# Optimization experiments

Measured on AMD Instinct MI355X. Metric: run time of the kernel, lower is better.

Reference implementation:

```python
import jax, jax.numpy as jnp
import numpy as np

B, T, HOR, N = 32, 12, 12, 883
D = 10      # embed_dim == time_dim
HID = 64    # rnn_units
OUT = 1     # output_dim
K = 2       # cheb_k: supports [I, A]


def _pdg2(x, e1, e2, E, Wp, bp):
    # x:[B,N,Ci]  e1,e2:[B,N,D]  E:[N,D]  Wp:[D,K,Ci,Co]  bp:[D,Co]
    nv1 = jnp.tanh(E[None] * e1)                      # [B,N,D]
    nv2 = jnp.tanh(E[None] * e2)
    A = jax.nn.softmax(jax.nn.relu(jnp.einsum('bnd,bmd->bnm', nv1, nv2)), axis=-1)
    xg = jnp.stack([x, jnp.einsum('bnm,bmc->bnc', A, x)], axis=2)   # [B,N,K,Ci]
    W = jnp.einsum('bnd,dkio->bnkio', nv1, Wp)        # node/time-adaptive weights
    b = jnp.einsum('bnd,do->bno', nv1, bp)
    return jnp.einsum('bnki,bnkio->bno', xg, W) + b


def _cell(x, h, e1, e2, E, gW, gb, uW, ub):
    xs = jnp.concatenate([x, h], axis=-1)
    zr = jax.nn.sigmoid(_pdg2(xs, e1, e2, E, gW, gb))
    z, r = jnp.split(zr, 2, axis=-1)
    cand = jnp.concatenate([x, z * h], axis=-1)
    hc = jnp.tanh(_pdg2(cand, e1, e2, E, uW, ub))
    return r * h + (1.0 - r) * hc


def setup_inputs() -> dict:
    key = jax.random.key(0)
    ks = jax.random.split(key, 20)
    s = 0.1
    inp = {
        'src_vals': jax.random.normal(ks[0], (B, T, N, 1), jnp.float32),
        'node_emb': s * jax.random.normal(ks[1], (N, D), jnp.float32),
        'tid_emb1': s * jax.random.normal(ks[2], (288, D), jnp.float32),
        'tid_emb2': s * jax.random.normal(ks[3], (288, D), jnp.float32),
        'diw_emb1': s * jax.random.normal(ks[4], (7, D), jnp.float32),
        'diw_emb2': s * jax.random.normal(ks[5], (7, D), jnp.float32),
        'enc_gate_W': s * jax.random.normal(ks[6], (D, K, 1 + HID, 2 * HID), jnp.float32),
        'enc_gate_b': s * jax.random.normal(ks[7], (D, 2 * HID), jnp.float32),
        'enc_upd_W': s * jax.random.normal(ks[8], (D, K, 1 + HID, HID), jnp.float32),
        'enc_upd_b': s * jax.random.normal(ks[9], (D, HID), jnp.float32),
        'dec_gate_W': s * jax.random.normal(ks[10], (D, K, OUT + HID, 2 * HID), jnp.float32),
        'dec_gate_b': s * jax.random.normal(ks[11], (D, 2 * HID), jnp.float32),
        'dec_upd_W': s * jax.random.normal(ks[12], (D, K, OUT + HID, HID), jnp.float32),
        'dec_upd_b': s * jax.random.normal(ks[13], (D, HID), jnp.float32),
        'proj_W': s * jax.random.normal(ks[14], (OUT, HID), jnp.float32),
        'proj_b': jnp.zeros((OUT,), jnp.float32),
        'src_tid': jax.random.randint(ks[15], (B, T, N), 0, 288, jnp.int32),
        'src_diw': jax.random.randint(ks[16], (B, T, N), 0, 7, jnp.int32),
        'tgt_tid': jax.random.randint(ks[17], (B, HOR, N), 0, 288, jnp.int32),
        'tgt_diw': jax.random.randint(ks[18], (B, HOR, N), 0, 7, jnp.int32),
    }
    return inp


def reference(src_vals, node_emb, tid_emb1, tid_emb2, diw_emb1, diw_emb2,
              enc_gate_W, enc_gate_b, enc_upd_W, enc_upd_b,
              dec_gate_W, dec_gate_b, dec_upd_W, dec_upd_b,
              proj_W, proj_b, src_tid, src_diw, tgt_tid, tgt_diw):
    tm = lambda a: jnp.swapaxes(a, 0, 1)   # batch-major -> time-major
    # periodic embeddings (use_week=True -> elementwise product)
    e1_en = tid_emb1[src_tid] * diw_emb1[src_diw]   # [B,T,N,D]
    e2_en = tid_emb2[src_tid] * diw_emb2[src_diw]
    e1_de = tid_emb1[tgt_tid] * diw_emb1[tgt_diw]   # [B,HOR,N,D]
    e2_de = tid_emb2[tgt_tid] * diw_emb2[tgt_diw]

    h0 = jnp.zeros((src_vals.shape[0], node_emb.shape[0], HID), src_vals.dtype)

    def enc_step(h, inp):
        x, e1, e2 = inp
        h = _cell(x, h, e1, e2, node_emb, enc_gate_W, enc_gate_b, enc_upd_W, enc_upd_b)
        return h, None

    h, _ = jax.lax.scan(enc_step, h0, (tm(src_vals), tm(e1_en), tm(e2_en)))

    go0 = jnp.zeros((src_vals.shape[0], node_emb.shape[0], OUT), src_vals.dtype)

    def dec_step(carry, inp):
        h, go = carry
        e1, e2 = inp
        h = _cell(go, h, e1, e2, node_emb, dec_gate_W, dec_gate_b, dec_upd_W, dec_upd_b)
        go = h @ proj_W.T + proj_b
        return (h, go), go

    _, outs = jax.lax.scan(dec_step, (h, go0), (tm(e1_de), tm(e2_de)))
    return jnp.swapaxes(outs, 0, 1)   # [B,HOR,N,OUT]
```

## Files before the change

### kernel.cpp

```cpp
#include <hip/hip_runtime.h>

#define BB 32
#define TSRC 12
#define HORZ 12
#define NN 883
#define DD 10
#define HH 64
#define BN (BB*NN)
#define BNP 28288
#define KF 5
#define NT 14

typedef __attribute__((ext_vector_type(8))) short short8;
typedef __attribute__((ext_vector_type(4))) float f32x4;

static __device__ __forceinline__ float sigmf(float x) { return 1.f/(1.f + __expf(-x)); }
static __device__ __forceinline__ float tanh_fast(float x) {
  float e = __expf(2.f*x);
  return (e - 1.f) / (e + 1.f);
}
static __device__ __forceinline__ unsigned int bf_hi(float f) {
  unsigned int u = __float_as_uint(f);
  return (u + 0x7fffu + ((u >> 16) & 1u)) >> 16;
}
static __device__ __forceinline__ float bf_f(unsigned int h) {
  return __uint_as_float(h << 16);
}
static __device__ __forceinline__ void lds_load16(const void* g, void* l) {
  __builtin_amdgcn_global_load_lds(
      (const __attribute__((address_space(1))) void*)g,
      (__attribute__((address_space(3))) void*)l, 16, 0, 0);
}

static __device__ __forceinline__ void swz_block(int& b, int& rt) {
  int lin = blockIdx.x + blockIdx.y*NT;
  int c = lin & 7, q = lin >> 3;
  b = c + ((q/NT) << 3);
  rt = q - (q/NT)*NT;
}

static __device__ __forceinline__ void xs_store(unsigned short* chunk, int c, int mm2, float v) {
  int p0 = (c*128 + (mm2 ^ ((c & 7) << 4))) >> 1;
  unsigned int hi = bf_hi(v);
  chunk[p0] = (unsigned short)hi;
  chunk[p0 + 4096] = (unsigned short)bf_hi(v - bf_f(hi));
}

__global__ __launch_bounds__(256) void prep_kernel(
    const float* __restrict__ tidE1, const float* __restrict__ tidE2,
    const float* __restrict__ diwE1, const float* __restrict__ diwE2,
    const float* __restrict__ nodeE,
    const int* __restrict__ tididx, const int* __restrict__ diwidx,
    const float* __restrict__ xsrc, int xmode, int t, int tlen,
    float* __restrict__ nv1T, float* __restrict__ nv2T,
    unsigned short* __restrict__ XsH, unsigned short* __restrict__ XsZ)
{
  int i = blockIdx.x*256 + threadIdx.x;
  if (i >= BN) return;
  int b = i / NN, n = i - b*NN;
  int gi = (b*tlen + t)*NN + n;
  int ti = tididx[gi]*DD, di = diwidx[gi]*DD;
  int nE = n*DD;
#pragma unroll
  for (int d = 0; d < DD; ++d) {
    float E = nodeE[nE+d];
    nv1T[d*BNP+i] = tanh_fast(E * (tidE1[ti+d] * diwE1[di+d]));
    nv2T[d*BNP+i] = tanh_fast(E * (tidE2[ti+d] * diwE2[di+d]));
  }
  float xv = (xmode == 0) ? xsrc[gi] : xsrc[i];
  size_t cb = ((size_t)(b*NT + (n >> 6)))*8192;
  int mm = n & 63;
  unsigned int hi = bf_hi(xv);
  unsigned short los = (unsigned short)bf_hi(xv - bf_f(hi));
  XsH[cb + mm] = (unsigned short)hi; XsH[cb + 4096 + mm] = los;
  XsZ[cb + mm] = (unsigned short)hi; XsZ[cb + 4096 + mm] = los;
}

__global__ __launch_bounds__(256) void wsplit_kernel(
    const float* __restrict__ W, const float* __restrict__ bias,
    int NO, unsigned short* __restrict__ Wf)
{
  int i = blockIdx.x*256 + threadIdx.x;
  int total = DD*2*KF*4*NO*8;
  if (i >= total) return;
  int j = i & 7; int r = i >> 3;
  int o = r % NO; r /= NO;
  int quad = r & 3; r >>= 2;
  int kf = r % KF; r /= KF;
  int hl = r & 1; int d = r >> 1;
  int kk = kf*32 + quad*8 + j;
  float v = 0.f;
  if (kk <= 64)       v = W[(size_t)(d*130 + kk)*NO + o];
  else if (kk == 65)  v = bias[d*NO + o];
  else if (kk <= 130) v = W[(size_t)(d*130 + kk - 1)*NO + o];
  unsigned int hi = bf_hi(v);
  Wf[i] = (hl == 0) ? (unsigned short)hi : (unsigned short)bf_hi(v - bf_f(hi));
}


__global__ __launch_bounds__(256,3) void attn_gate(
    const float* __restrict__ nv1T, const float* __restrict__ nv2T,
    const unsigned short* __restrict__ Xs,
    const float* __restrict__ h,
    const unsigned short* __restrict__ Wf,
    float* __restrict__ rbuf,
    unsigned short* __restrict__ XsZ, float* __restrict__ zh63)
{
  __shared__ float nv1s[DD][64];
  __shared__ float linv[64];
  __shared__ alignas(16) unsigned char U[46080];
  unsigned short* XT = (unsigned short*)U;
  unsigned short* PT = (unsigned short*)(U + 16384);
  float* nv2s = (float*)(U + 34816);
  float* xcolb = (float*)(U + 39936);
  int b, rt;
  swz_block(b, rt);
  int r0 = rt*64;
  int tid = threadIdx.x;
  int rg = tid >> 4, cg = tid & 15;
  int base = b*NN;
  int lane = tid & 63, lm = lane & 15, quad = lane >> 4;
  int w = tid >> 6, mp = w >> 1, np = w & 1;
  const unsigned short* XsB = Xs + (size_t)b*NT*8192;

  for (int idx = tid; idx < DD*64; idx += 256) {
    int d = idx >> 6, r = idx & 63;
    nv1s[d][r] = (r0 + r < NN) ? nv1T[d*BNP + base + r0 + r] : 0.f;
  }

  int4 xt[4];
  float nvr[3]; float xcr;
  {
    const int4* s0 = (const int4*)XsB;
#pragma unroll
    for (int i = 0; i < 4; ++i) xt[i] = s0[w*64 + lane + i*256];
#pragma unroll
    for (int i = 0; i < 3; ++i) {
      int idx = tid + i*256; float v = 0.f;
      if (idx < DD*64) { int d = idx>>6, m = idx&63; v = (m < NN) ? nv2T[d*BNP + base + m] : 0.f; }
      nvr[i] = v;
    }
    xcr = (tid < 64 && tid < NN) ? h[(size_t)63*BNP + base + tid] : 0.f;
#pragma unroll
    for (int i = 0; i < 4; ++i)
      *(int4*)((char*)XT + w*1024 + lane*16 + i*4096) = xt[i];
#pragma unroll
    for (int i = 0; i < 3; ++i) {
      int idx = tid + i*256;
      if (idx < DD*64) nv2s[idx] = nvr[i];
    }
    if (tid < 64) xcolb[tid] = xcr;
  }
  __syncthreads();

  f32x4 accv[2][2] = {};
  float acclp[4] = {}, acc5p[4] = {};

  for (int tI = 0; tI < NT; ++tI) {
    int cur = tI & 1, nxt = cur ^ 1;
    int m0 = tI*64, m0n = m0 + 64;
    bool hasn = tI < NT-1;
    if (hasn) {
      const int4* src = (const int4*)(XsB + (size_t)(tI+1)*8192);
#pragma unroll
      for (int i = 0; i < 4; ++i) xt[i] = src[w*64 + lane + i*256];
#pragma unroll
      for (int i = 0; i < 3; ++i) {
        int idx = tid + i*256; float v = 0.f;
        if (idx < DD*64) { int d = idx>>6, m = idx&63; v = (m0n + m < NN) ? nv2T[d*BNP + base + m0n + m] : 0.f; }
        nvr[i] = v;
      }
      xcr = (tid < 64 && m0n + tid < NN) ? h[(size_t)63*BNP + base + m0n + tid] : 0.f;
    }
    float s[4][4] = {};
#pragma unroll
    for (int d = 0; d < DD; ++d) {
      float4 a4 = *(const float4*)&nv1s[d][rg*4];
      float4 c4 = *(const float4*)&nv2s[cur*(DD*64) + d*64 + cg*4];
      const float* ap = (const float*)&a4;
      const float* cp = (const float*)&c4;
#pragma unroll
      for (int j = 0; j < 4; ++j)
#pragma unroll
        for (int jj = 0; jj < 4; ++jj)
          s[j][jj] += ap[j]*cp[jj];
    }
    int mvlim = NN - m0;
    float ev[4][4];
#pragma unroll
    for (int jj = 0; jj < 4; ++jj) {
      int m = cg*4 + jj;
      float xm = xcolb[cur*64 + m];
      bool okm = m < mvlim;
#pragma unroll
      for (int j = 0; j < 4; ++j) {
        float e = okm ? __expf(fmaxf(s[j][jj], 0.f)) : 0.f;
        ev[j][jj] = e;
        acclp[j] += e;
        acc5p[j] = fmaf(e, xm, acc5p[j]);
      }
    }
    {
      unsigned int* P1 = (unsigned int*)PT;
      unsigned int* P2 = (unsigned int*)(PT + 64*72);
#pragma unroll
      for (int j = 0; j < 4; ++j) {
        int r = rg*4 + j;
        unsigned int h0 = bf_hi(ev[j][0]), h1 = bf_hi(ev[j][1]), h2 = bf_hi(ev[j][2]), h3 = bf_hi(ev[j][3]);
        unsigned int l0 = bf_hi(ev[j][0]-bf_f(h0)), l1 = bf_hi(ev[j][1]-bf_f(h1));
        unsigned int l2 = bf_hi(ev[j][2]-bf_f(h2)), l3 = bf_hi(ev[j][3]-bf_f(h3));
        int dw = r*36 + cg*2;
        P1[dw] = h0 | (h1 << 16); P1[dw+1] = h2 | (h3 << 16);
        P2[dw] = l0 | (l1 << 16); P2[dw+1] = l2 | (l3 << 16);
      }
    }
    __syncthreads();
    {
      short8 Aa[2][2], Ab[2][2], Ba[2][2], Bb[2][2];
#pragma unroll
      for (int mt = 0; mt < 2; ++mt) {
        int r = mp*32 + mt*16 + lm;
#pragma unroll
        for (int kf = 0; kf < 2; ++kf) {
          Aa[mt][kf] = *(const short8*)&PT[r*72 + quad*8 + kf*32];
          Ab[mt][kf] = *(const short8*)&PT[64*72 + r*72 + quad*8 + kf*32];
        }
      }
#pragma unroll
      for (int ntl = 0; ntl < 2; ++ntl) {
        int c = np*32 + ntl*16 + lm;
        int swz = (c & 7) << 4;
        int cb0 = c*128 + quad*16;
#pragma unroll
        for (int kf = 0; kf < 2; ++kf) {
          int a = (cb0 + kf*64) ^ swz;
          Ba[ntl][kf] = *(const short8*)((const char*)XT + a);
          Bb[ntl][kf] = *(const short8*)((const char*)XT + a + 8192);
        }
      }
#pragma unroll
      for (int kf = 0; kf < 2; ++kf)
#pragma unroll
        for (int mt = 0; mt < 2; ++mt)
#pragma unroll
          for (int ntl = 0; ntl < 2; ++ntl) {
            accv[mt][ntl] = __builtin_amdgcn_mfma_f32_16x16x32_bf16(Aa[mt][kf], Ba[ntl][kf], accv[mt][ntl], 0,0,0);
            accv[mt][ntl] = __builtin_amdgcn_mfma_f32_16x16x32_bf16(Aa[mt][kf], Bb[ntl][kf], accv[mt][ntl], 0,0,0);
            accv[mt][ntl] = __builtin_amdgcn_mfma_f32_16x16x32_bf16(Ab[mt][kf], Ba[ntl][kf], accv[mt][ntl], 0,0,0);
          }
    }
    if (hasn) {
#pragma unroll
      for (int i = 0; i < 3; ++i) {
        int idx = tid + i*256;
        if (idx < DD*64) nv2s[nxt*(DD*64) + idx] = nvr[i];
      }
      if (tid < 64) xcolb[nxt*64 + tid] = xcr;
    }
    __syncthreads();
    if (hasn) {
#pragma unroll
      for (int i = 0; i < 4; ++i)
        *(int4*)((char*)XT + w*1024 + lane*16 + i*4096) = xt[i];
    }
  }
  int mrow_x = tid >> 2, ksub = tid & 3;
  int gmx = base + r0 + mrow_x;
  const unsigned short* chk_in = Xs + (size_t)(b*NT + rt)*8192;
  int mm2x = mrow_x*2;
  unsigned int pjh[9], pjl[9];
  {
    float r63v = h[(size_t)63*BNP + gmx];
    unsigned int h63 = bf_hi(r63v);
    unsigned int l63 = bf_hi(r63v - bf_f(h63));
#pragma unroll
    for (int i = 0; i < 9; ++i) {
      int kk = ksub*2 + 8*i;
      unsigned int h0 = 0, l0 = 0, h1 = 0, l1 = 0;
      if (kk <= 63) {
        int idx = (kk*128 + (mm2x ^ ((kk & 7) << 4))) >> 1;
        h0 = chk_in[idx]; l0 = chk_in[idx + 4096];
      } else if (kk == 64) { h0 = h63; l0 = l63; }
      int k1 = kk + 1;
      if (kk <= 62) {
        int idx1 = (k1*128 + (mm2x ^ ((k1 & 7) << 4))) >> 1;
        h1 = chk_in[idx1]; l1 = chk_in[idx1 + 4096];
      } else if (k1 == 65) { h1 = 0x3F80u; l1 = 0u; }
      pjh[i] = h0 | (h1 << 16);
      pjl[i] = l0 | (l1 << 16);
    }
  }
#pragma unroll
  for (int off = 1; off <= 8; off <<= 1)
#pragma unroll
    for (int j = 0; j < 4; ++j) {
      acclp[j] += __shfl_xor(acclp[j], off, 64);
      acc5p[j] += __shfl_xor(acc5p[j], off, 64);
    }
  __syncthreads();
  {
    unsigned int* Z = (unsigned int*)(U + 36864);
    for (int idx = tid; idx < 2304; idx += 256) Z[idx] = 0;
  }
  __syncthreads();
  unsigned short* XA = (unsigned short*)U;
  if (cg == 0) {
#pragma unroll
    for (int j = 0; j < 4; ++j) {
      float li = 1.f / acclp[j];
      int r = rg*4 + j;
      linv[r] = li;
      float v = acc5p[j]*li;
      unsigned int hi = bf_hi(v);
      XA[(4*64 + r)*72 + 2] = (unsigned short)hi;
      XA[(4*64 + r)*72 + 32 + 2] = (unsigned short)bf_hi(v - bf_f(hi));
    }
  }
  __syncthreads();
#pragma unroll
  for (int mt = 0; mt < 2; ++mt) {
    int rbase = mp*32 + mt*16 + quad*4;
    float4 lv = *(const float4*)&linv[rbase];
    const float* lvp = (const float*)&lv;
#pragma unroll
    for (int ntl = 0; ntl < 2; ++ntl) {
      int c = np*32 + ntl*16 + lm;
      int kk = 66 + c;
      int kf = kk >> 5, kkl = kk & 31;
#pragma unroll
      for (int r4 = 0; r4 < 4; ++r4) {
        float v = accv[mt][ntl][r4] * lvp[r4];
        unsigned int hi = bf_hi(v);
        int p = (kf*64 + rbase + r4)*72 + kkl;
        XA[p] = (unsigned short)hi;
        XA[p + 32] = (unsigned short)bf_hi(v - bf_f(hi));
      }
    }
  }
  {
    unsigned int* X1 = (unsigned int*)U;
#pragma unroll
    for (int i = 0; i < 9; ++i) {
      int kk = ksub*2 + 8*i;
      if (kk > 64) continue;
      int kf = kk >> 5, kkl = kk & 31;
      int dw = (kf*64 + mrow_x)*36 + (kkl >> 1);
      X1[dw] = pjh[i];
      X1[dw + 16] = pjl[i];
    }
  }
  __syncthreads();
  short8 A1[2][KF], A2[2][KF];
#pragma unroll
  for (int mt = 0; mt < 2; ++mt) {
    int mrow = mp*32 + mt*16 + lm;
#pragma unroll
    for (int kf = 0; kf < KF; ++kf) {
      A1[mt][kf] = *(const short8*)&XA[(kf*64 + mrow)*72 + quad*8];
      A2[mt][kf] = *(const short8*)&XA[(kf*64 + mrow)*72 + 32 + quad*8];
    }
  }
  __syncthreads();
  unsigned char* bufA = U;
  unsigned char* bufB = U + 20480;
  const int colb = np*32 + lm;
#pragma unroll 1
  for (int co = 0; co < 2; ++co) {
    int co0 = co*64;
    {
      const unsigned short* src = Wf + ((size_t)(w*5)*128 + co0)*8 + lane*8;
#pragma unroll
      for (int i = 0; i < 5; ++i)
        lds_load16(src + (size_t)i*128*8, bufA + (w*5+i)*1024);
    }
    f32x4 accO[2][2] = {};
#pragma unroll 1
    for (int d = 0; d < DD; ++d) {
      f32x4 td[2][2] = {};
      __syncthreads();
      {
        const unsigned short* src = Wf + ((size_t)((d*2+1)*20 + w*5)*128 + co0)*8 + lane*8;
#pragma unroll
        for (int i = 0; i < 5; ++i)
          lds_load16(src + (size_t)i*128*8, bufB + (w*5+i)*1024);
      }
#pragma unroll
      for (int kf = 0; kf < KF; ++kf) {
        int cb = ((kf*4 + quad)*64 + colb)*16;
#pragma unroll
        for (int ntl = 0; ntl < 2; ++ntl) {
          short8 Bh = *(const short8*)(bufA + cb + ntl*256);
          td[0][ntl] = __builtin_amdgcn_mfma_f32_16x16x32_bf16(A1[0][kf], Bh, td[0][ntl], 0,0,0);
          td[0][ntl] = __builtin_amdgcn_mfma_f32_16x16x32_bf16(A2[0][kf], Bh, td[0][ntl], 0,0,0);
          td[1][ntl] = __builtin_amdgcn_mfma_f32_16x16x32_bf16(A1[1][kf], Bh, td[1][ntl], 0,0,0);
          td[1][ntl] = __builtin_amdgcn_mfma_f32_16x16x32_bf16(A2[1][kf], Bh, td[1][ntl], 0,0,0);
        }
      }
      __syncthreads();
      if (d < DD-1) {
        const unsigned short* src = Wf + ((size_t)((d+1)*2*20 + w*5)*128 + co0)*8 + lane*8;
#pragma unroll
        for (int i = 0; i < 5; ++i)
          lds_load16(src + (size_t)i*128*8, bufA + (w*5+i)*1024);
      }
#pragma unroll
      for (int kf = 0; kf < KF; ++kf) {
        int cb = ((kf*4 + quad)*64 + colb)*16;
#pragma unroll
        for (int ntl = 0; ntl < 2; ++ntl) {
          short8 Bl = *(const short8*)(bufB + cb + ntl*256);
          td[0][ntl] = __builtin_amdgcn_mfma_f32_16x16x32_bf16(A1[0][kf], Bl, td[0][ntl], 0,0,0);
          td[1][ntl] = __builtin_amdgcn_mfma_f32_16x16x32_bf16(A1[1][kf], Bl, td[1][ntl], 0,0,0);
        }
      }
#pragma unroll
      for (int mt = 0; mt < 2; ++mt) {
        float4 nv4 = *(const float4*)&nv1s[d][mp*32 + mt*16 + quad*4];
        const float* nvp = (const float*)&nv4;
#pragma unroll
        for (int ntl = 0; ntl < 2; ++ntl)
#pragma unroll
          for (int r = 0; r < 4; ++r)
            accO[mt][ntl][r] += nvp[r] * td[mt][ntl][r];
      }
    }
    float* CT = (float*)U;
    __syncthreads();
#pragma unroll
    for (int mt = 0; mt < 2; ++mt)
#pragma unroll
      for (int ntl = 0; ntl < 2; ++ntl)
#pragma unroll
        for (int r = 0; r < 4; ++r)
          CT[(mp*32 + mt*16 + quad*4 + r)*67 + np*32 + ntl*16 + lm] = accO[mt][ntl][r];
    __syncthreads();
    {
      int mm = tid & 63, og = tid >> 6;
      int n = r0 + mm;
      int gm = base + n;
      bool okn = n < NN;
      if (co == 0) {
        unsigned short* chk = XsZ + ((size_t)(b*NT + rt))*8192;
        int mm2 = mm*2;
        for (int j = 0; j < 16; ++j) {
          int o = og*16 + j;
          float z = sigmf(CT[mm*67 + o]);
          float zhv = z * h[(size_t)o*BNP + gm];
          if (okn) {
            if (o < 63) xs_store(chk, o + 1, mm2, zhv);
            else zh63[gm] = zhv;
          }
        }
      } else {
        for (int j = 0; j < 16; ++j) {
          int o = og*16 + j;
          if (okn) rbuf[(size_t)o*BNP + gm] = sigmf(CT[mm*67 + o]);
        }
      }
    }
    __syncthreads();
  }
}

__global__ __launch_bounds__(256,3) void attn_upd(
    const float* __restrict__ nv1T, const float* __restrict__ nv2T,
    const unsigned short* __restrict__ Xs,
    const float* __restrict__ zh63,
    float* __restrict__ hstate,
    const unsigned short* __restrict__ Wf,
    const float* __restrict__ rbuf,
    int dec, const float* __restrict__ pW, const float* __restrict__ pb,
    float* __restrict__ go, float* __restrict__ dout,
    unsigned short* __restrict__ XsH, int t)
{
  __shared__ float nv1s[DD][64];
  __shared__ float linv[64];
  __shared__ alignas(16) unsigned char U[46080];
  unsigned short* XT = (unsigned short*)U;
  unsigned short* PT = (unsigned short*)(U + 16384);
  float* nv2s = (float*)(U + 34816);
  float* xcolb = (float*)(U + 39936);
  int b, rt;
  swz_block(b, rt);
  int r0 = rt*64;
  int tid = threadIdx.x;
  int rg = tid >> 4, cg = tid & 15;
  int base = b*NN;
  int lane = tid & 63, lm = lane & 15, quad = lane >> 4;
  int w = tid >> 6, mp = w >> 1, np = w & 1;
  const unsigned short* XsB = Xs + (size_t)b*NT*8192;

  for (int idx = tid; idx < DD*64; idx += 256) {
    int d = idx >> 6, r = idx & 63;
    nv1s[d][r] = (r0 + r < NN) ? nv1T[d*BNP + base + r0 + r] : 0.f;
  }

  int4 xt[4];
  float nvr[3]; float xcr;
  {
    const int4* s0 = (const int4*)XsB;
#pragma unroll
    for (int i = 0; i < 4; ++i) xt[i] = s0[w*64 + lane + i*256];
#pragma unroll
    for (int i = 0; i < 3; ++i) {
      int idx = tid + i*256; float v = 0.f;
      if (idx < DD*64) { int d = idx>>6, m = idx&63; v = (m < NN) ? nv2T[d*BNP + base + m] : 0.f; }
      nvr[i] = v;
    }
    xcr = (tid < 64 && tid < NN) ? zh63[base + tid] : 0.f;
#pragma unroll
    for (int i = 0; i < 4; ++i)
      *(int4*)((char*)XT + w*1024 + lane*16 + i*4096) = xt[i];
#pragma unroll
    for (int i = 0; i < 3; ++i) {
      int idx = tid + i*256;
      if (idx < DD*64) nv2s[idx] = nvr[i];
    }
    if (tid < 64) xcolb[tid] = xcr;
  }
  __syncthreads();

  f32x4 accv[2][2] = {};
  float acclp[4] = {}, acc5p[4] = {};

  for (int tI = 0; tI < NT; ++tI) {
    int cur = tI & 1, nxt = cur ^ 1;
    int m0 = tI*64, m0n = m0 + 64;
    bool hasn = tI < NT-1;
    if (hasn) {
      const int4* src = (const int4*)(XsB + (size_t)(tI+1)*8192);
#pragma unroll
      for (int i = 0; i < 4; ++i) xt[i] = src[w*64 + lane + i*256];
#pragma unroll
      for (int i = 0; i < 3; ++i) {
        int idx = tid + i*256; float v = 0.f;
        if (idx < DD*64) { int d = idx>>6, m = idx&63; v = (m0n + m < NN) ? nv2T[d*BNP + base + m0n + m] : 0.f; }
        nvr[i] = v;
      }
      xcr = (tid < 64 && m0n + tid < NN) ? zh63[base + m0n + tid] : 0.f;
    }
    float s[4][4] = {};
#pragma unroll
    for (int d = 0; d < DD; ++d) {
      float4 a4 = *(const float4*)&nv1s[d][rg*4];
      float4 c4 = *(const float4*)&nv2s[cur*(DD*64) + d*64 + cg*4];
      const float* ap = (const float*)&a4;
      const float* cp = (const float*)&c4;
#pragma unroll
      for (int j = 0; j < 4; ++j)
#pragma unroll
        for (int jj = 0; jj < 4; ++jj)
          s[j][jj] += ap[j]*cp[jj];
    }
    int mvlim = NN - m0;
    float ev[4][4];
#pragma unroll
    for (int jj = 0; jj < 4; ++jj) {
      int m = cg*4 + jj;
      float xm = xcolb[cur*64 + m];
      bool okm = m < mvlim;
#pragma unroll
      for (int j = 0; j < 4; ++j) {
        float e = okm ? __expf(fmaxf(s[j][jj], 0.f)) : 0.f;
        ev[j][jj] = e;
        acclp[j] += e;
        acc5p[j] = fmaf(e, xm, acc5p[j]);
      }
    }
    {
      unsigned int* P1 = (unsigned int*)PT;
      unsigned int* P2 = (unsigned int*)(PT + 64*72);
#pragma unroll
      for (int j = 0; j < 4; ++j) {
        int r = rg*4 + j;
        unsigned int h0 = bf_hi(ev[j][0]), h1 = bf_hi(ev[j][1]), h2 = bf_hi(ev[j][2]), h3 = bf_hi(ev[j][3]);
        unsigned int l0 = bf_hi(ev[j][0]-bf_f(h0)), l1 = bf_hi(ev[j][1]-bf_f(h1));
        unsigned int l2 = bf_hi(ev[j][2]-bf_f(h2)), l3 = bf_hi(ev[j][3]-bf_f(h3));
        int dw = r*36 + cg*2;
        P1[dw] = h0 | (h1 << 16); P1[dw+1] = h2 | (h3 << 16);
        P2[dw] = l0 | (l1 << 16); P2[dw+1] = l2 | (l3 << 16);
      }
    }
    __syncthreads();
    {
      short8 Aa[2][2], Ab[2][2], Ba[2][2], Bb[2][2];
#pragma unroll
      for (int mt = 0; mt < 2; ++mt) {
        int r = mp*32 + mt*16 + lm;
#pragma unroll
        for (int kf = 0; kf < 2; ++kf) {
          Aa[mt][kf] = *(const short8*)&PT[r*72 + quad*8 + kf*32];
          Ab[mt][kf] = *(const short8*)&PT[64*72 + r*72 + quad*8 + kf*32];
        }
      }
#pragma unroll
      for (int ntl = 0; ntl < 2; ++ntl) {
        int c = np*32 + ntl*16 + lm;
        int swz = (c & 7) << 4;
        int cb0 = c*128 + quad*16;
#pragma unroll
        for (int kf = 0; kf < 2; ++kf) {
          int a = (cb0 + kf*64) ^ swz;
          Ba[ntl][kf] = *(const short8*)((const char*)XT + a);
          Bb[ntl][kf] = *(const short8*)((const char*)XT + a + 8192);
        }
      }
#pragma unroll
      for (int kf = 0; kf < 2; ++kf)
#pragma unroll
        for (int mt = 0; mt < 2; ++mt)
#pragma unroll
          for (int ntl = 0; ntl < 2; ++ntl) {
            accv[mt][ntl] = __builtin_amdgcn_mfma_f32_16x16x32_bf16(Aa[mt][kf], Ba[ntl][kf], accv[mt][ntl], 0,0,0);
            accv[mt][ntl] = __builtin_amdgcn_mfma_f32_16x16x32_bf16(Aa[mt][kf], Bb[ntl][kf], accv[mt][ntl], 0,0,0);
            accv[mt][ntl] = __builtin_amdgcn_mfma_f32_16x16x32_bf16(Ab[mt][kf], Ba[ntl][kf], accv[mt][ntl], 0,0,0);
          }
    }
    if (hasn) {
#pragma unroll
      for (int i = 0; i < 3; ++i) {
        int idx = tid + i*256;
        if (idx < DD*64) nv2s[nxt*(DD*64) + idx] = nvr[i];
      }
      if (tid < 64) xcolb[nxt*64 + tid] = xcr;
    }
    __syncthreads();
    if (hasn) {
#pragma unroll
      for (int i = 0; i < 4; ++i)
        *(int4*)((char*)XT + w*1024 + lane*16 + i*4096) = xt[i];
    }
  }
  int mrow_x = tid >> 2, ksub = tid & 3;
  int gmx = base + r0 + mrow_x;
  const unsigned short* chk_in = Xs + (size_t)(b*NT + rt)*8192;
  int mm2x = mrow_x*2;
  unsigned int pjh[9], pjl[9];
  {
    float r63v = zh63[gmx];
    unsigned int h63 = bf_hi(r63v);
    unsigned int l63 = bf_hi(r63v - bf_f(h63));
#pragma unroll
    for (int i = 0; i < 9; ++i) {
      int kk = ksub*2 + 8*i;
      unsigned int h0 = 0, l0 = 0, h1 = 0, l1 = 0;
      if (kk <= 63) {
        int idx = (kk*128 + (mm2x ^ ((kk & 7) << 4))) >> 1;
        h0 = chk_in[idx]; l0 = chk_in[idx + 4096];
      } else if (kk == 64) { h0 = h63; l0 = l63; }
      int k1 = kk + 1;
      if (kk <= 62) {
        int idx1 = (k1*128 + (mm2x ^ ((k1 & 7) << 4))) >> 1;
        h1 = chk_in[idx1]; l1 = chk_in[idx1 + 4096];
      } else if (k1 == 65) { h1 = 0x3F80u; l1 = 0u; }
      pjh[i] = h0 | (h1 << 16);
      pjl[i] = l0 | (l1 << 16);
    }
  }
#pragma unroll
  for (int off = 1; off <= 8; off <<= 1)
#pragma unroll
    for (int j = 0; j < 4; ++j) {
      acclp[j] += __shfl_xor(acclp[j], off, 64);
      acc5p[j] += __shfl_xor(acc5p[j], off, 64);
    }
  __syncthreads();
  {
    unsigned int* Z = (unsigned int*)(U + 36864);
    for (int idx = tid; idx < 2304; idx += 256) Z[idx] = 0;
  }
  __syncthreads();
  unsigned short* XA = (unsigned short*)U;
  if (cg == 0) {
#pragma unroll
    for (int j = 0; j < 4; ++j) {
      float li = 1.f / acclp[j];
      int r = rg*4 + j;
      linv[r] = li;
      float v = acc5p[j]*li;
      unsigned int hi = bf_hi(v);
      XA[(4*64 + r)*72 + 2] = (unsigned short)hi;
      XA[(4*64 + r)*72 + 32 + 2] = (unsigned short)bf_hi(v - bf_f(hi));
    }
  }
  __syncthreads();
#pragma unroll
  for (int mt = 0; mt < 2; ++mt) {
    int rbase = mp*32 + mt*16 + quad*4;
    float4 lv = *(const float4*)&linv[rbase];
    const float* lvp = (const float*)&lv;
#pragma unroll
    for (int ntl = 0; ntl < 2; ++ntl) {
      int c = np*32 + ntl*16 + lm;
      int kk = 66 + c;
      int kf = kk >> 5, kkl = kk & 31;
#pragma unroll
      for (int r4 = 0; r4 < 4; ++r4) {
        float v = accv[mt][ntl][r4] * lvp[r4];
        unsigned int hi = bf_hi(v);
        int p = (kf*64 + rbase + r4)*72 + kkl;
        XA[p] = (unsigned short)hi;
        XA[p + 32] = (unsigned short)bf_hi(v - bf_f(hi));
      }
    }
  }
  {
    unsigned int* X1 = (unsigned int*)U;
#pragma unroll
    for (int i = 0; i < 9; ++i) {
      int kk = ksub*2 + 8*i;
      if (kk > 64) continue;
      int kf = kk >> 5, kkl = kk & 31;
      int dw = (kf*64 + mrow_x)*36 + (kkl >> 1);
      X1[dw] = pjh[i];
      X1[dw + 16] = pjl[i];
    }
  }
  __syncthreads();
  short8 A1[2][KF], A2[2][KF];
#pragma unroll
  for (int mt = 0; mt < 2; ++mt) {
    int mrow = mp*32 + mt*16 + lm;
#pragma unroll
    for (int kf = 0; kf < KF; ++kf) {
      A1[mt][kf] = *(const short8*)&XA[(kf*64 + mrow)*72 + quad*8];
      A2[mt][kf] = *(const short8*)&XA[(kf*64 + mrow)*72 + 32 + quad*8];
    }
  }
  __syncthreads();
  unsigned char* bufA = U;
  unsigned char* bufB = U + 20480;
  const int colb = np*32 + lm;
  {
    const unsigned short* src = Wf + (size_t)(w*5)*64*8 + lane*8;
#pragma unroll
    for (int i = 0; i < 5; ++i)
      lds_load16(src + (size_t)i*64*8, bufA + (w*5+i)*1024);
  }
  f32x4 accO[2][2] = {};
#pragma unroll 1
  for (int d = 0; d < DD; ++d) {
    f32x4 td[2][2] = {};
    __syncthreads();
    {
      const unsigned short* src = Wf + (size_t)((d*2+1)*20 + w*5)*64*8 + lane*8;
#pragma unroll
      for (int i = 0; i < 5; ++i)
        lds_load16(src + (size_t)i*64*8, bufB + (w*5+i)*1024);
    }
#pragma unroll
    for (int kf = 0; kf < KF; ++kf) {
      int cb = ((kf*4 + quad)*64 + colb)*16;
#pragma unroll
      for (int ntl = 0; ntl < 2; ++ntl) {
        short8 Bh = *(const short8*)(bufA + cb + ntl*256);
        td[0][ntl] = __builtin_amdgcn_mfma_f32_16x16x32_bf16(A1[0][kf], Bh, td[0][ntl], 0,0,0);
        td[0][ntl] = __builtin_amdgcn_mfma_f32_16x16x32_bf16(A2[0][kf], Bh, td[0][ntl], 0,0,0);
        td[1][ntl] = __builtin_amdgcn_mfma_f32_16x16x32_bf16(A1[1][kf], Bh, td[1][ntl], 0,0,0);
        td[1][ntl] = __builtin_amdgcn_mfma_f32_16x16x32_bf16(A2[1][kf], Bh, td[1][ntl], 0,0,0);
      }
    }
    __syncthreads();
    if (d < DD-1) {
      const unsigned short* src = Wf + (size_t)((d+1)*2*20 + w*5)*64*8 + lane*8;
#pragma unroll
      for (int i = 0; i < 5; ++i)
        lds_load16(src + (size_t)i*64*8, bufA + (w*5+i)*1024);
    }
#pragma unroll
    for (int kf = 0; kf < KF; ++kf) {
      int cb = ((kf*4 + quad)*64 + colb)*16;
#pragma unroll
      for (int ntl = 0; ntl < 2; ++ntl) {
        short8 Bl = *(const short8*)(bufB + cb + ntl*256);
        td[0][ntl] = __builtin_amdgcn_mfma_f32_16x16x32_bf16(A1[0][kf], Bl, td[0][ntl], 0,0,0);
        td[1][ntl] = __builtin_amdgcn_mfma_f32_16x16x32_bf16(A1[1][kf], Bl, td[1][ntl], 0,0,0);
      }
    }
#pragma unroll
    for (int mt = 0; mt < 2; ++mt) {
      float4 nv4 = *(const float4*)&nv1s[d][mp*32 + mt*16 + quad*4];
      const float* nvp = (const float*)&nv4;
#pragma unroll
      for (int ntl = 0; ntl < 2; ++ntl)
#pragma unroll
        for (int r = 0; r < 4; ++r)
          accO[mt][ntl][r] += nvp[r] * td[mt][ntl][r];
    }
  }
  float* CT = (float*)U;
  __syncthreads();
#pragma unroll
  for (int mt = 0; mt < 2; ++mt)
#pragma unroll
    for (int ntl = 0; ntl < 2; ++ntl)
#pragma unroll
      for (int r = 0; r < 4; ++r)
        CT[(mp*32 + mt*16 + quad*4 + r)*67 + np*32 + ntl*16 + lm] = accO[mt][ntl][r];
  __syncthreads();
  {
    int mm = tid & 63, og = tid >> 6;
    int n = r0 + mm;
    int gm = base + n;
    bool okn = n < NN;
    unsigned short* chk = XsH + ((size_t)(b*NT + rt))*8192;
    int mm2 = mm*2;
    float pp = 0.f;
    for (int j = 0; j < 16; ++j) {
      int o = og*16 + j;
      float hc = tanhf(CT[mm*67 + o]);
      float r = rbuf[(size_t)o*BNP + gm];
      float hv = hstate[(size_t)o*BNP + gm];
      float hn = r*hv + (1.f - r)*hc;
      if (okn) {
        hstate[(size_t)o*BNP + gm] = hn;
        if (o < 63) xs_store(chk, o + 1, mm2, hn);
      }
      if (dec) pp = fmaf(hn, pW[o], pp);
    }
    if (dec) {
      float* PS = CT + 64*67;
      __syncthreads();
      PS[mm*4 + og] = pp;
      __syncthreads();
      if (tid < 64) {
        int n2 = r0 + tid;
        if (n2 < NN) {
          float s = pb[0] + PS[tid*4] + PS[tid*4+1] + PS[tid*4+2] + PS[tid*4+3];
          go[base + n2] = s;
          dout[(b*HORZ + t)*NN + n2] = s;
        }
      }
    }
  }
}

extern "C" void kernel_launch(void* const* d_in, const int* in_sizes, int n_in,
                              void* d_out, int out_size, void* d_ws, size_t ws_size,
                              hipStream_t stream) {
  (void)in_sizes; (void)n_in; (void)out_size; (void)ws_size;
  const float* src_vals = (const float*)d_in[0];
  const float* node_emb = (const float*)d_in[1];
  const float* tid1 = (const float*)d_in[2];
  const float* tid2 = (const float*)d_in[3];
  const float* diw1 = (const float*)d_in[4];
  const float* diw2 = (const float*)d_in[5];
  const float* egW = (const float*)d_in[6];
  const float* egb = (const float*)d_in[7];
  const float* euW = (const float*)d_in[8];
  const float* eub = (const float*)d_in[9];
  const float* dgW = (const float*)d_in[10];
  const float* dgb = (const float*)d_in[11];
  const float* duW = (const float*)d_in[12];
  const float* dub = (const float*)d_in[13];
  const float* pW  = (const float*)d_in[14];
  const float* pb  = (const float*)d_in[15];
  const int* stid = (const int*)d_in[16];
  const int* sdiw = (const int*)d_in[17];
  const int* ttid = (const int*)d_in[18];
  const int* tdiw = (const int*)d_in[19];
  float* out = (float*)d_out;

  float* wp = (float*)d_ws;
  float* hbuf = wp; wp += (size_t)64*BNP;
  float* zh63 = wp; wp += BNP + 64;
  float* rbuf = wp; wp += (size_t)64*BNP;
  float* nv1T = wp; wp += (size_t)DD*BNP;
  float* nv2T = wp; wp += (size_t)DD*BNP;
  float* go   = wp; wp += BN + 64;
  unsigned short* egS = (unsigned short*)wp; wp += 204800;
  unsigned short* dgS = (unsigned short*)wp; wp += 204800;
  unsigned short* euS = (unsigned short*)wp; wp += 102400;
  unsigned short* duS = (unsigned short*)wp; wp += 102400;
  unsigned short* XsH = (unsigned short*)wp; wp += 1835008;
  unsigned short* XsZ = (unsigned short*)wp; wp += 1835008;

  hipMemsetAsync(hbuf, 0, sizeof(float)*(size_t)64*BNP, stream);
  hipMemsetAsync(go, 0, sizeof(float)*(BN+64), stream);
  hipMemsetAsync(XsH, 0, (size_t)BB*NT*16384, stream);
  hipMemsetAsync(XsZ, 0, (size_t)BB*NT*16384, stream);

  wsplit_kernel<<<1600,256,0,stream>>>(egW, egb, 128, egS);
  wsplit_kernel<<<1600,256,0,stream>>>(dgW, dgb, 128, dgS);
  wsplit_kernel<<<800,256,0,stream>>>(euW, eub, 64, euS);
  wsplit_kernel<<<800,256,0,stream>>>(duW, dub, 64, duS);

  dim3 fgrid(NT, BB);
  for (int t = 0; t < TSRC; ++t) {
    prep_kernel<<<111,256,0,stream>>>(tid1,tid2,diw1,diw2,node_emb,stid,sdiw,src_vals,0,t,TSRC,nv1T,nv2T,XsH,XsZ);
    attn_gate<<<fgrid,256,0,stream>>>(nv1T,nv2T,XsH,hbuf,egS,rbuf,XsZ,zh63);
    attn_upd<<<fgrid,256,0,stream>>>(nv1T,nv2T,XsZ,zh63,hbuf,euS,rbuf,0,pW,pb,go,out,XsH,t);
  }
  for (int t = 0; t < HORZ; ++t) {
    prep_kernel<<<111,256,0,stream>>>(tid1,tid2,diw1,diw2,node_emb,ttid,tdiw,go,1,t,HORZ,nv1T,nv2T,XsH,XsZ);
    attn_gate<<<fgrid,256,0,stream>>>(nv1T,nv2T,XsH,hbuf,dgS,rbuf,XsZ,zh63);
    attn_upd<<<fgrid,256,0,stream>>>(nv1T,nv2T,XsZ,zh63,hbuf,duS,rbuf,1,pW,pb,go,out,XsH,t);
  }
}
```

Measured before the change: 4.448 ms.

## Precompute all step embeddings in one launch and fold next-input staging into update kernel

Replaces the per-step prep kernel with a single batched launch that computes the tanh node/time embeddings for all 24 encoder and decoder steps into a larger workspace. Writing the next step's input x (source value, zero, or the decoder's own projected output) into the bf16 split staging buffers now happens at the end of attn_upd. This removes 24 small serial launches and their dependency bubbles, at the cost of extra workspace memory and some added work in the update kernel's epilogue. Correctness depends on the cross-step staging writes landing in the right buffers (XsH and XsZ share a region).

```diff
diff --git a/kernel.cpp b/kernel.cpp
--- a/kernel.cpp
+++ b/kernel.cpp
@@ -10,6 +10,7 @@
 #define BNP 28288
 #define KF 5
 #define NT 14
+#define NST (TSRC+HORZ)
 
 typedef __attribute__((ext_vector_type(8))) short short8;
 typedef __attribute__((ext_vector_type(4))) float f32x4;
@@ -46,34 +47,43 @@
   chunk[p0 + 4096] = (unsigned short)bf_hi(v - bf_f(hi));
 }
 
-__global__ __launch_bounds__(256) void prep_kernel(
+__global__ __launch_bounds__(256) void prep_all(
     const float* __restrict__ tidE1, const float* __restrict__ tidE2,
     const float* __restrict__ diwE1, const float* __restrict__ diwE2,
     const float* __restrict__ nodeE,
-    const int* __restrict__ tididx, const int* __restrict__ diwidx,
-    const float* __restrict__ xsrc, int xmode, int t, int tlen,
-    float* __restrict__ nv1T, float* __restrict__ nv2T,
+    const int* __restrict__ stid, const int* __restrict__ sdiw,
+    const int* __restrict__ ttid, const int* __restrict__ tdiw,
+    const float* __restrict__ xsrc,
+    float* __restrict__ nv1A, float* __restrict__ nv2A,
     unsigned short* __restrict__ XsH, unsigned short* __restrict__ XsZ)
 {
   int i = blockIdx.x*256 + threadIdx.x;
   if (i >= BN) return;
+  int st = blockIdx.y;
   int b = i / NN, n = i - b*NN;
-  int gi = (b*tlen + t)*NN + n;
-  int ti = tididx[gi]*DD, di = diwidx[gi]*DD;
+  const int* tix = (st < TSRC) ? stid : ttid;
+  const int* dix = (st < TSRC) ? sdiw : tdiw;
+  int t = (st < TSRC) ? st : st - TSRC;
+  int gi = (b*TSRC + t)*NN + n;
+  int ti = tix[gi]*DD, di = dix[gi]*DD;
   int nE = n*DD;
+  float* nv1T = nv1A + (size_t)st*DD*BNP;
+  float* nv2T = nv2A + (size_t)st*DD*BNP;
 #pragma unroll
   for (int d = 0; d < DD; ++d) {
     float E = nodeE[nE+d];
     nv1T[d*BNP+i] = tanh_fast(E * (tidE1[ti+d] * diwE1[di+d]));
     nv2T[d*BNP+i] = tanh_fast(E * (tidE2[ti+d] * diwE2[di+d]));
   }
-  float xv = (xmode == 0) ? xsrc[gi] : xsrc[i];
-  size_t cb = ((size_t)(b*NT + (n >> 6)))*8192;
-  int mm = n & 63;
-  unsigned int hi = bf_hi(xv);
-  unsigned short los = (unsigned short)bf_hi(xv - bf_f(hi));
-  XsH[cb + mm] = (unsigned short)hi; XsH[cb + 4096 + mm] = los;
-  XsZ[cb + mm] = (unsigned short)hi; XsZ[cb + 4096 + mm] = los;
+  if (st == 0) {
+    float xv = xsrc[gi];
+    size_t cb = ((size_t)(b*NT + (n >> 6)))*8192;
+    int mm = n & 63;
+    unsigned int hi = bf_hi(xv);
+    unsigned short los = (unsigned short)bf_hi(xv - bf_f(hi));
+    XsH[cb + mm] = (unsigned short)hi; XsH[cb + 4096 + mm] = los;
+    XsZ[cb + mm] = (unsigned short)hi; XsZ[cb + 4096 + mm] = los;
+  }
 }
 
 __global__ __launch_bounds__(256) void wsplit_kernel(
@@ -471,7 +481,9 @@
     const float* __restrict__ rbuf,
     int dec, const float* __restrict__ pW, const float* __restrict__ pb,
     float* __restrict__ go, float* __restrict__ dout,
-    unsigned short* __restrict__ XsH, int t)
+    unsigned short* __restrict__ XsH, int t,
+    const float* __restrict__ xsrc, int xnmode, int xnt,
+    unsigned short* __restrict__ XsZm)
 {
   __shared__ float nv1s[DD][64];
   __shared__ float linv[64];
@@ -806,6 +818,7 @@
     unsigned short* chk = XsH + ((size_t)(b*NT + rt))*8192;
     int mm2 = mm*2;
     float pp = 0.f;
+    float sval = 0.f;
     for (int j = 0; j < 16; ++j) {
       int o = og*16 + j;
       float hc = tanhf(CT[mm*67 + o]);
@@ -829,6 +842,24 @@
           float s = pb[0] + PS[tid*4] + PS[tid*4+1] + PS[tid*4+2] + PS[tid*4+3];
           go[base + n2] = s;
           dout[(b*HORZ + t)*NN + n2] = s;
+          sval = s;
+        }
+      }
+    }
+    if (xnmode) {
+      if (tid < 64) {
+        int n2 = r0 + tid;
+        if (n2 < NN) {
+          float xn;
+          if (xnmode == 1)      xn = xsrc[(b*TSRC + xnt)*NN + n2];
+          else if (xnmode == 2) xn = 0.f;
+          else                  xn = sval;
+          unsigned int hix = bf_hi(xn);
+          unsigned short lox = (unsigned short)bf_hi(xn - bf_f(hix));
+          unsigned short* cH = XsH + ((size_t)(b*NT + rt))*8192;
+          unsigned short* cZ = XsZm + ((size_t)(b*NT + rt))*8192;
+          cH[tid] = (unsigned short)hix; cH[4096 + tid] = lox;
+          cZ[tid] = (unsigned short)hix; cZ[4096 + tid] = lox;
         }
       }
     }
@@ -865,8 +896,8 @@
   float* hbuf = wp; wp += (size_t)64*BNP;
   float* zh63 = wp; wp += BNP + 64;
   float* rbuf = wp; wp += (size_t)64*BNP;
-  float* nv1T = wp; wp += (size_t)DD*BNP;
-  float* nv2T = wp; wp += (size_t)DD*BNP;
+  float* nv1A = wp; wp += (size_t)NST*DD*BNP;
+  float* nv2A = wp; wp += (size_t)NST*DD*BNP;
   float* go   = wp; wp += BN + 64;
   unsigned short* egS = (unsigned short*)wp; wp += 204800;
   unsigned short* dgS = (unsigned short*)wp; wp += 204800;
@@ -885,15 +916,22 @@
   wsplit_kernel<<<800,256,0,stream>>>(euW, eub, 64, euS);
   wsplit_kernel<<<800,256,0,stream>>>(duW, dub, 64, duS);
 
+  dim3 pgrid(111, NST);
+  prep_all<<<pgrid,256,0,stream>>>(tid1,tid2,diw1,diw2,node_emb,stid,sdiw,ttid,tdiw,src_vals,nv1A,nv2A,XsH,XsZ);
+
   dim3 fgrid(NT, BB);
   for (int t = 0; t < TSRC; ++t) {
-    prep_kernel<<<111,256,0,stream>>>(tid1,tid2,diw1,diw2,node_emb,stid,sdiw,src_vals,0,t,TSRC,nv1T,nv2T,XsH,XsZ);
-    attn_gate<<<fgrid,256,0,stream>>>(nv1T,nv2T,XsH,hbuf,egS,rbuf,XsZ,zh63);
-    attn_upd<<<fgrid,256,0,stream>>>(nv1T,nv2T,XsZ,zh63,hbuf,euS,rbuf,0,pW,pb,go,out,XsH,t);
+    const float* n1 = nv1A + (size_t)t*DD*BNP;
+    const float* n2 = nv2A + (size_t)t*DD*BNP;
+    attn_gate<<<fgrid,256,0,stream>>>(n1,n2,XsH,hbuf,egS,rbuf,XsZ,zh63);
+    int xnm = (t < TSRC-1) ? 1 : 2;
+    attn_upd<<<fgrid,256,0,stream>>>(n1,n2,XsZ,zh63,hbuf,euS,rbuf,0,pW,pb,go,out,XsH,t,src_vals,xnm,t+1,XsZ);
   }
   for (int t = 0; t < HORZ; ++t) {
-    prep_kernel<<<111,256,0,stream>>>(tid1,tid2,diw1,diw2,node_emb,ttid,tdiw,go,1,t,HORZ,nv1T,nv2T,XsH,XsZ);
-    attn_gate<<<fgrid,256,0,stream>>>(nv1T,nv2T,XsH,hbuf,dgS,rbuf,XsZ,zh63);
-    attn_upd<<<fgrid,256,0,stream>>>(nv1T,nv2T,XsZ,zh63,hbuf,duS,rbuf,1,pW,pb,go,out,XsH,t);
-  }
-}
+    const float* n1 = nv1A + (size_t)(TSRC+t)*DD*BNP;
+    const float* n2 = nv2A + (size_t)(TSRC+t)*DD*BNP;
+    attn_gate<<<fgrid,256,0,stream>>>(n1,n2,XsH,hbuf,dgS,rbuf,XsZ,zh63);
+    int xnm = (t < HORZ-1) ? 3 : 0;
+    attn_upd<<<fgrid,256,0,stream>>>(n1,n2,XsZ,zh63,hbuf,duS,rbuf,1,pW,pb,go,out,XsH,t,src_vals,xnm,0,XsZ);
+  }
+}
```

Measured after the change: 4.376 ms, median of 3. Within noise of the previous version (-1.6%).
